# Kernel tuning notes

Hardware: AMD Instinct MI355X
Metric: run time of the kernel (lower is better)

Reference implementation:

```python
import jax, jax.numpy as jnp
import numpy as np

DIM = 33
B, H, W = 16, 1024, 1024


def _identity_lut(dim):
    v = jnp.arange(dim, dtype=jnp.float32) / (dim - 1)
    # buffer[0,i,j,k]=R varies with k, [1]=G with j, [2]=B with i
    r = jnp.broadcast_to(v[None, None, :], (dim, dim, dim))
    g = jnp.broadcast_to(v[None, :, None], (dim, dim, dim))
    b = jnp.broadcast_to(v[:, None, None], (dim, dim, dim))
    return jnp.stack([r, g, b], axis=0)  # (3, dim, dim, dim)


def setup_inputs() -> dict:
    key = jax.random.key(0)
    kx, = jax.random.split(key, 1)
    x = jax.random.uniform(kx, (B, 3, H, W), dtype=jnp.float32)  # RGB in [0,1)
    lut = _identity_lut(DIM)
    return {"x": x, "lut": lut}


def _trilerp(lut, x):
    # lut: (3, dim, dim, dim); x: (B, 3, H, W) in [0,1)
    dim = lut.shape[-1]
    binsize = 1.000001 / (dim - 1)
    lutf = lut.reshape(3, -1)                      # (3, dim^3)
    r, g, b = x[:, 0], x[:, 1], x[:, 2]            # each (B,H,W)
    rs, gs, bs = r / binsize, g / binsize, b / binsize
    rid = jnp.floor(rs).astype(jnp.int32)
    gid = jnp.floor(gs).astype(jnp.int32)
    bid = jnp.floor(bs).astype(jnp.int32)
    rd = rs - rid                                   # fractional parts
    gd = gs - gid
    bd = bs - bid
    base = rid + gid * dim + bid * dim * dim        # flat index, r fastest
    out = jnp.zeros_like(x)
    for dr in (0, 1):
        wr = rd if dr else (1.0 - rd)
        for dg in (0, 1):
            wg = gd if dg else (1.0 - gd)
            for db in (0, 1):
                wb = bd if db else (1.0 - bd)
                w = wr * wg * wb                    # (B,H,W)
                idx = base + dr + dg * dim + db * dim * dim
                corner = lutf[:, idx]               # (3,B,H,W) gather
                out = out + w[:, None] * jnp.transpose(corner, (1, 0, 2, 3))
    return out


def reference(x, lut):
    return _trilerp(lut, x)
```

## Files before the change

### kernel.cpp

```cpp
#include <hip/hip_runtime.h>

#define DIM 33
#define DIM2 (DIM * DIM)
#define NLUT (DIM * DIM * DIM)
#define NLUT_PAD 35940

typedef float        v4f __attribute__((ext_vector_type(4)));
typedef unsigned int v4u __attribute__((ext_vector_type(4)));

__device__ __forceinline__ unsigned q8(float v) {
    float c = fminf(fmaxf(v, 0.0f), 1.0f);
    return (unsigned)(fmaf(c, 255.0f, 0.5f));
}

__global__ void repack_q8_kernel(const float* __restrict__ lut,
                                 unsigned* __restrict__ lutq) {
    int i = blockIdx.x * blockDim.x + threadIdx.x;
    if (i >= NLUT_PAD) return;
    int j = (i < NLUT) ? i : NLUT - 1;
    unsigned r = q8(lut[j]);
    unsigned g = q8(lut[NLUT + j]);
    unsigned b = q8(lut[2 * NLUT + j]);
    lutq[i] = r | (g << 8) | (b << 16);
}

struct f3 { float x, y, z; };

__device__ __forceinline__ f3 dec(unsigned u) {
    f3 o;
    o.x = (float)(u & 0xffu);
    o.y = (float)((u >> 8) & 0xffu);
    o.z = (float)((u >> 16) & 0xffu);
    return o;
}

__device__ __forceinline__ f3 lerp3(const f3 a, const f3 b, const float t) {
    f3 o;
    o.x = fmaf(t, b.x - a.x, a.x);
    o.y = fmaf(t, b.y - a.y, a.y);
    o.z = fmaf(t, b.z - a.z, a.z);
    return o;
}

__global__ __launch_bounds__(1024) void lut3d_apply_lds_kernel(
    const float* __restrict__ x, const unsigned* __restrict__ lutq,
    float* __restrict__ out) {
    constexpr int HW    = 1024 * 1024;
    constexpr int HW4   = HW / 4;
    constexpr int ITERS = 16;

    __shared__ unsigned ls[NLUT_PAD];

    {
        const v4u* src = reinterpret_cast<const v4u*>(lutq);
        v4u* dst = reinterpret_cast<v4u*>(ls);
        for (int i = threadIdx.x; i < NLUT_PAD / 4; i += 1024)
            dst[i] = src[i];
    }
    __syncthreads();

    const float inv_bin = 32.0f / 1.000001f;

    const int bi   = blockIdx.x;
    const int bimg = bi >> 4;
    const int off0 = (bi & 15) * (ITERS * 1024) + threadIdx.x;
    const v4f* xb = reinterpret_cast<const v4f*>(x + (size_t)bimg * 3 * HW) + off0;
    v4f*       ob = reinterpret_cast<v4f*>(out + (size_t)bimg * 3 * HW) + off0;

    v4f pr[3][3];
#pragma unroll
    for (int p = 0; p < 2; ++p) {
        pr[p][0] = xb[p * 1024];
        pr[p][1] = xb[p * 1024 + HW4];
        pr[p][2] = xb[p * 1024 + 2 * HW4];
    }

#pragma unroll
    for (int it = 0; it < ITERS; ++it) {
        const int s0 = it % 3, s2 = (it + 2) % 3;
        if (it + 2 < ITERS) {
            pr[s2][0] = xb[(it + 2) * 1024];
            pr[s2][1] = xb[(it + 2) * 1024 + HW4];
            pr[s2][2] = xb[(it + 2) * 1024 + 2 * HW4];
        }

        v4f cr = pr[s0][0], cg = pr[s0][1], cb = pr[s0][2];

        float rd[4], gd[4], bd[4];
        unsigned C[4][8];

#pragma unroll
        for (int k = 0; k < 4; ++k) {
            float rs = cr[k] * inv_bin;
            float gs = cg[k] * inv_bin;
            float bs = cb[k] * inv_bin;
            float rf = floorf(rs), gf = floorf(gs), bf = floorf(bs);
            rd[k] = rs - rf;
            gd[k] = gs - gf;
            bd[k] = bs - bf;

            float idxf = fmaf(1089.0f, bf, fmaf(33.0f, gf, rf));
            int idx = (int)idxf;

            C[k][0] = ls[idx];
            C[k][1] = ls[idx + 1];
            C[k][2] = ls[idx + DIM];
            C[k][3] = ls[idx + DIM + 1];
            C[k][4] = ls[idx + DIM2];
            C[k][5] = ls[idx + DIM2 + 1];
            C[k][6] = ls[idx + DIM2 + DIM];
            C[k][7] = ls[idx + DIM2 + DIM + 1];
        }

        v4f or4, og4, ob4;

#pragma unroll
        for (int k = 0; k < 4; ++k) {
            f3 a00 = lerp3(dec(C[k][0]), dec(C[k][1]), rd[k]);
            f3 a10 = lerp3(dec(C[k][2]), dec(C[k][3]), rd[k]);
            f3 a01 = lerp3(dec(C[k][4]), dec(C[k][5]), rd[k]);
            f3 a11 = lerp3(dec(C[k][6]), dec(C[k][7]), rd[k]);
            f3 m0  = lerp3(a00, a10, gd[k]);
            f3 m1  = lerp3(a01, a11, gd[k]);
            f3 res = lerp3(m0, m1, bd[k]);
            or4[k] = res.x * (1.0f / 255.0f);
            og4[k] = res.y * (1.0f / 255.0f);
            ob4[k] = res.z * (1.0f / 255.0f);
        }

        __builtin_nontemporal_store(or4, ob + it * 1024);
        __builtin_nontemporal_store(og4, ob + it * 1024 + HW4);
        __builtin_nontemporal_store(ob4, ob + it * 1024 + 2 * HW4);
    }
}

extern "C" void kernel_launch(void* const* d_in, const int* in_sizes, int n_in,
                              void* d_out, int out_size, void* d_ws, size_t ws_size,
                              hipStream_t stream) {
    const float* x   = (const float*)d_in[0];
    const float* lut = (const float*)d_in[1];
    float* out       = (float*)d_out;

    unsigned* lutq = (unsigned*)d_ws;

    repack_q8_kernel<<<(NLUT_PAD + 255) / 256, 256, 0, stream>>>(lut, lutq);
    lut3d_apply_lds_kernel<<<256, 1024, 0, stream>>>(x, lutq, out);
}
```

Before: 74.36 us.

## Software-pipeline LUT gathers across half-iterations and pack RG lerps into v2f

Splits each iteration's four pixels into two halves and interleaves the LDS corner gathers for one half with the interpolation math of the other, including prefetching the next iteration's first half. This aims to hide LDS latency behind ALU work. It also packs the red and green lerps into 2-wide float vectors so the compiler can emit packed FMA instructions. The cost is higher register pressure at 1024 threads per block, which could force spills.

```diff
diff --git a/kernel.cpp b/kernel.cpp
--- a/kernel.cpp
+++ b/kernel.cpp
@@ -6,6 +6,7 @@
 #define NLUT_PAD 35940
 
 typedef float        v4f __attribute__((ext_vector_type(4)));
+typedef float        v2f __attribute__((ext_vector_type(2)));
 typedef unsigned int v4u __attribute__((ext_vector_type(4)));
 
 __device__ __forceinline__ unsigned q8(float v) {
@@ -24,22 +25,68 @@
     lutq[i] = r | (g << 8) | (b << 16);
 }
 
-struct f3 { float x, y, z; };
+struct c3 { v2f rg; float b; };
 
-__device__ __forceinline__ f3 dec(unsigned u) {
-    f3 o;
-    o.x = (float)(u & 0xffu);
-    o.y = (float)((u >> 8) & 0xffu);
-    o.z = (float)((u >> 16) & 0xffu);
+__device__ __forceinline__ c3 dec(unsigned u) {
+    c3 o;
+    o.rg.x = (float)(u & 0xffu);
+    o.rg.y = (float)((u >> 8) & 0xffu);
+    o.b    = (float)((u >> 16) & 0xffu);
     return o;
 }
 
-__device__ __forceinline__ f3 lerp3(const f3 a, const f3 b, const float t) {
-    f3 o;
-    o.x = fmaf(t, b.x - a.x, a.x);
-    o.y = fmaf(t, b.y - a.y, a.y);
-    o.z = fmaf(t, b.z - a.z, a.z);
+__device__ __forceinline__ c3 lerp3(const c3 a, const c3 b, const float t) {
+    c3 o;
+    v2f t2 = {t, t};
+    o.rg = t2 * (b.rg - a.rg) + a.rg;
+    o.b  = fmaf(t, b.b - a.b, a.b);
     return o;
+}
+
+__device__ __forceinline__ void issue2(const unsigned* __restrict__ ls,
+                                       const v4f cr, const v4f cg, const v4f cb,
+                                       int k0, float* rd, float* gd, float* bd,
+                                       unsigned C[2][8]) {
+    const float inv_bin = 32.0f / 1.000001f;
+#pragma unroll
+    for (int k = 0; k < 2; ++k) {
+        float rs = cr[k0 + k] * inv_bin;
+        float gs = cg[k0 + k] * inv_bin;
+        float bs = cb[k0 + k] * inv_bin;
+        float rf = floorf(rs), gf = floorf(gs), bf = floorf(bs);
+        rd[k] = rs - rf;
+        gd[k] = gs - gf;
+        bd[k] = bs - bf;
+        float idxf = fmaf(1089.0f, bf, fmaf(33.0f, gf, rf));
+        int idx = (int)idxf;
+        C[k][0] = ls[idx];
+        C[k][1] = ls[idx + 1];
+        C[k][2] = ls[idx + DIM];
+        C[k][3] = ls[idx + DIM + 1];
+        C[k][4] = ls[idx + DIM2];
+        C[k][5] = ls[idx + DIM2 + 1];
+        C[k][6] = ls[idx + DIM2 + DIM];
+        C[k][7] = ls[idx + DIM2 + DIM + 1];
+    }
+}
+
+__device__ __forceinline__ void comp2(const float* rd, const float* gd, const float* bd,
+                                      const unsigned C[2][8], int k0,
+                                      v4f& or4, v4f& og4, v4f& ob4) {
+#pragma unroll
+    for (int k = 0; k < 2; ++k) {
+        c3 a00 = lerp3(dec(C[k][0]), dec(C[k][1]), rd[k]);
+        c3 a10 = lerp3(dec(C[k][2]), dec(C[k][3]), rd[k]);
+        c3 a01 = lerp3(dec(C[k][4]), dec(C[k][5]), rd[k]);
+        c3 a11 = lerp3(dec(C[k][6]), dec(C[k][7]), rd[k]);
+        c3 m0  = lerp3(a00, a10, gd[k]);
+        c3 m1  = lerp3(a01, a11, gd[k]);
+        c3 res = lerp3(m0, m1, bd[k]);
+        v2f s = res.rg * (1.0f / 255.0f);
+        or4[k0 + k] = s.x;
+        og4[k0 + k] = s.y;
+        ob4[k0 + k] = res.b * (1.0f / 255.0f);
+    }
 }
 
 __global__ __launch_bounds__(1024) void lut3d_apply_lds_kernel(
@@ -59,8 +106,6 @@
     }
     __syncthreads();
 
-    const float inv_bin = 32.0f / 1.000001f;
-
     const int bi   = blockIdx.x;
     const int bimg = bi >> 4;
     const int off0 = (bi & 15) * (ITERS * 1024) + threadIdx.x;
@@ -75,9 +120,14 @@
         pr[p][2] = xb[p * 1024 + 2 * HW4];
     }
 
+    float rdA[2], gdA[2], bdA[2], rdB[2], gdB[2], bdB[2];
+    unsigned CA[2][8], CB[2][8];
+
+    issue2(ls, pr[0][0], pr[0][1], pr[0][2], 0, rdA, gdA, bdA, CA);
+
 #pragma unroll
     for (int it = 0; it < ITERS; ++it) {
-        const int s0 = it % 3, s2 = (it + 2) % 3;
+        const int s0 = it % 3, s1 = (it + 1) % 3, s2 = (it + 2) % 3;
         if (it + 2 < ITERS) {
             pr[s2][0] = xb[(it + 2) * 1024];
             pr[s2][1] = xb[(it + 2) * 1024 + HW4];
@@ -86,47 +136,15 @@
 
         v4f cr = pr[s0][0], cg = pr[s0][1], cb = pr[s0][2];
 
-        float rd[4], gd[4], bd[4];
-        unsigned C[4][8];
-
-#pragma unroll
-        for (int k = 0; k < 4; ++k) {
-            float rs = cr[k] * inv_bin;
-            float gs = cg[k] * inv_bin;
-            float bs = cb[k] * inv_bin;
-            float rf = floorf(rs), gf = floorf(gs), bf = floorf(bs);
-            rd[k] = rs - rf;
-            gd[k] = gs - gf;
-            bd[k] = bs - bf;
-
-            float idxf = fmaf(1089.0f, bf, fmaf(33.0f, gf, rf));
-            int idx = (int)idxf;
-
-            C[k][0] = ls[idx];
-            C[k][1] = ls[idx + 1];
-            C[k][2] = ls[idx + DIM];
-            C[k][3] = ls[idx + DIM + 1];
-            C[k][4] = ls[idx + DIM2];
-            C[k][5] = ls[idx + DIM2 + 1];
-            C[k][6] = ls[idx + DIM2 + DIM];
-            C[k][7] = ls[idx + DIM2 + DIM + 1];
-        }
+        issue2(ls, cr, cg, cb, 2, rdB, gdB, bdB, CB);
 
         v4f or4, og4, ob4;
+        comp2(rdA, gdA, bdA, CA, 0, or4, og4, ob4);
 
-#pragma unroll
-        for (int k = 0; k < 4; ++k) {
-            f3 a00 = lerp3(dec(C[k][0]), dec(C[k][1]), rd[k]);
-            f3 a10 = lerp3(dec(C[k][2]), dec(C[k][3]), rd[k]);
-            f3 a01 = lerp3(dec(C[k][4]), dec(C[k][5]), rd[k]);
-            f3 a11 = lerp3(dec(C[k][6]), dec(C[k][7]), rd[k]);
-            f3 m0  = lerp3(a00, a10, gd[k]);
-            f3 m1  = lerp3(a01, a11, gd[k]);
-            f3 res = lerp3(m0, m1, bd[k]);
-            or4[k] = res.x * (1.0f / 255.0f);
-            og4[k] = res.y * (1.0f / 255.0f);
-            ob4[k] = res.z * (1.0f / 255.0f);
-        }
+        if (it + 1 < ITERS)
+            issue2(ls, pr[s1][0], pr[s1][1], pr[s1][2], 0, rdA, gdA, bdA, CA);
+
+        comp2(rdB, gdB, bdB, CB, 2, or4, og4, ob4);
 
         __builtin_nontemporal_store(or4, ob + it * 1024);
         __builtin_nontemporal_store(og4, ob + it * 1024 + HW4);
```

New measurement: 75.10 us. No clear change (+1.0%).
